# Kernel tuning notes

Hardware: AMD Instinct MI355X
Metric: run time of the kernel (lower is better)

## Reference

```python
import jax, jax.numpy as jnp
import numpy as np

B, T, Q, D = 8192, 65, 20, 100  # batch, tweet len, question len, 2*hidden_dim


def setup_inputs() -> dict:
    key = jax.random.key(0)
    kH, kU, k1, k2, k3 = jax.random.split(key, 5)
    # Ws params are a single normal row repeated across the length dim
    ws1 = jnp.tile(jax.random.normal(k1, (1, D), dtype=jnp.float32), (T, 1))
    ws2 = jnp.tile(jax.random.normal(k2, (1, D), dtype=jnp.float32), (Q, 1))
    ws3 = jnp.tile(jax.random.normal(k3, (1, D), dtype=jnp.float32), (T, 1))
    return {
        "H": jax.random.normal(kH, (B, T, D), dtype=jnp.float32),
        "U": jax.random.normal(kU, (B, Q, D), dtype=jnp.float32),
        "Ws1": ws1,
        "Ws2": ws2,
        "Ws3": ws3,
    }


def reference(H, U, Ws1, Ws2, Ws3):
    # H: [B,T,D], U: [B,Q,D]
    H1 = jnp.sum(H * Ws1, axis=2)[:, :, None]        # [B,T,1]
    U1 = jnp.sum(U * Ws2, axis=2)[:, None, :]        # [B,1,Q]
    HU = jnp.einsum('btd,bqd->btq', H * Ws3, U)      # [B,T,Q]
    S = H1 + U1 + HU                                 # [B,T,Q]
    at = jax.nn.softmax(S, axis=2)                   # attend tweet->question
    Util = jnp.einsum('btq,bqd->btd', at, U)         # [B,T,D]
    beta = jnp.max(S, axis=2)                        # [B,T]
    b = jax.nn.softmax(beta, axis=1)[:, :, None]     # [B,T,1]
    Htil = jnp.sum(b * H, axis=1)[:, None, :]        # [B,1,D] broadcast over T
    G = jnp.concatenate((H, Util, H * Util, H * Htil), axis=2)  # [B,T,4D]
    return G
```

## Files before the change

kernel.cpp:

```cpp
#include <hip/hip_runtime.h>
#include <math.h>

#define NB 8192
#define T 65
#define Q 20
#define D 100
#define D4 25
#define SP 24
#define SP4 6

__global__ __launch_bounds__(256) void attn_fused_kernel(
    const float* __restrict__ Hg,
    const float* __restrict__ Ug,
    const float* __restrict__ Ws1,
    const float* __restrict__ Ws2,
    const float* __restrict__ Ws3,
    float* __restrict__ Gg)
{
    __shared__ float4 sH4[T*D4];
    __shared__ float4 sU4[Q*D4];
    __shared__ float4 sU3e4[(Q+1)*D4];
    __shared__ float4 sS4[T*SP4];
    __shared__ float4 sHtilP[4][D4];
    __shared__ float4 sU1q4[5];
    __shared__ float  sH1[T];
    __shared__ float  sBeta[T];
    __shared__ float  sBsm[T];

    const int b   = blockIdx.x;
    const int tid = threadIdx.x;
    const float4* Hb = (const float4*)(Hg + (size_t)b * (T*D));
    const float4* Ub = (const float4*)(Ug + (size_t)b * (Q*D));
    float* sSf = (float*)sS4;

    for (int i = tid; i < T*D4; i += 256) sH4[i] = Hb[i];
    {
        const float4* w3g = (const float4*)Ws3;
        for (int i = tid; i < Q*D4; i += 256) {
            const float4 u = Ub[i];
            sU4[i] = u;
            const int dd = i - (i/D4)*D4;
            const float4 w = w3g[dd];
            float4 v; v.x=u.x*w.x; v.y=u.y*w.y; v.z=u.z*w.z; v.w=u.w*w.w;
            sU3e4[i] = v;
        }
        if (tid < D4) sU3e4[Q*D4 + tid] = ((const float4*)Ws1)[tid];
    }
    __syncthreads();

    if (tid < 119) {
        const int tg = tid / 7;
        const int jg = tid - tg*7;
        int rb0 = ((tg*4 + 0) < T ? (tg*4 + 0) : T-1) * D4;
        int rb1 = ((tg*4 + 1) < T ? (tg*4 + 1) : T-1) * D4;
        int rb2 = ((tg*4 + 2) < T ? (tg*4 + 2) : T-1) * D4;
        int rb3 = ((tg*4 + 3) < T ? (tg*4 + 3) : T-1) * D4;
        float acc[4][3];
        #pragma unroll
        for (int i = 0; i < 4; ++i)
            #pragma unroll
            for (int k = 0; k < 3; ++k) acc[i][k] = 0.f;
        #pragma unroll 5
        for (int d4 = 0; d4 < D4; ++d4) {
            float4 h0 = sH4[rb0 + d4];
            float4 h1 = sH4[rb1 + d4];
            float4 h2 = sH4[rb2 + d4];
            float4 h3 = sH4[rb3 + d4];
            #pragma unroll
            for (int k = 0; k < 3; ++k) {
                const float4 w = sU3e4[(jg*3+k)*D4 + d4];
                acc[0][k] = fmaf(h0.x, w.x, acc[0][k]); acc[0][k] = fmaf(h0.y, w.y, acc[0][k]);
                acc[0][k] = fmaf(h0.z, w.z, acc[0][k]); acc[0][k] = fmaf(h0.w, w.w, acc[0][k]);
                acc[1][k] = fmaf(h1.x, w.x, acc[1][k]); acc[1][k] = fmaf(h1.y, w.y, acc[1][k]);
                acc[1][k] = fmaf(h1.z, w.z, acc[1][k]); acc[1][k] = fmaf(h1.w, w.w, acc[1][k]);
                acc[2][k] = fmaf(h2.x, w.x, acc[2][k]); acc[2][k] = fmaf(h2.y, w.y, acc[2][k]);
                acc[2][k] = fmaf(h2.z, w.z, acc[2][k]); acc[2][k] = fmaf(h2.w, w.w, acc[2][k]);
                acc[3][k] = fmaf(h3.x, w.x, acc[3][k]); acc[3][k] = fmaf(h3.y, w.y, acc[3][k]);
                acc[3][k] = fmaf(h3.z, w.z, acc[3][k]); acc[3][k] = fmaf(h3.w, w.w, acc[3][k]);
            }
        }
        #pragma unroll
        for (int i = 0; i < 4; ++i) {
            const int t = tg*4 + i;
            if (t < T) {
                #pragma unroll
                for (int k = 0; k < 3; ++k) {
                    const int cc = jg*3 + k;
                    if (cc < Q) sSf[t*SP + cc] = acc[i][k];
                    else        sH1[t] = acc[i][k];
                }
            }
        }
    } else if (tid >= 128 && tid < 128 + Q) {
        const int q = tid - 128;
        const float4* ur = sU4 + q*D4;
        const float4* w2 = (const float4*)Ws2;
        float acc = 0.f;
        #pragma unroll
        for (int k = 0; k < D4; ++k) {
            const float4 u = ur[k], w = w2[k];
            acc = fmaf(u.x, w.x, acc); acc = fmaf(u.y, w.y, acc);
            acc = fmaf(u.z, w.z, acc); acc = fmaf(u.w, w.w, acc);
        }
        ((float*)sU1q4)[q] = acc;
    }
    __syncthreads();

    if (tid < T) {
        const int t = tid;
        float4 r[5];
        #pragma unroll
        for (int c = 0; c < 5; ++c) {
            r[c] = sS4[t*SP4 + c];
            const float4 u1 = sU1q4[c];
            r[c].x += u1.x; r[c].y += u1.y; r[c].z += u1.z; r[c].w += u1.w;
        }
        float m = -1e30f;
        #pragma unroll
        for (int c = 0; c < 5; ++c)
            m = fmaxf(m, fmaxf(fmaxf(r[c].x, r[c].y), fmaxf(r[c].z, r[c].w)));
        float s = 0.f;
        #pragma unroll
        for (int c = 0; c < 5; ++c) {
            r[c].x = __expf(r[c].x - m); r[c].y = __expf(r[c].y - m);
            r[c].z = __expf(r[c].z - m); r[c].w = __expf(r[c].w - m);
            s += r[c].x + r[c].y + r[c].z + r[c].w;
        }
        const float inv = 1.f / s;
        #pragma unroll
        for (int c = 0; c < 5; ++c) {
            r[c].x *= inv; r[c].y *= inv; r[c].z *= inv; r[c].w *= inv;
            sS4[t*SP4 + c] = r[c];
        }
        sBeta[t] = sH1[t] + m;
    }
    __syncthreads();

    if (tid < 64) {
        const float v0 = sBeta[tid];
        const float v1 = (tid == 0) ? sBeta[64] : -1e30f;
        float mx = fmaxf(v0, v1);
        #pragma unroll
        for (int off = 32; off >= 1; off >>= 1)
            mx = fmaxf(mx, __shfl_xor(mx, off, 64));
        const float e0 = __expf(v0 - mx);
        const float e1 = (tid == 0) ? __expf(v1 - mx) : 0.f;
        float s = e0 + e1;
        #pragma unroll
        for (int off = 32; off >= 1; off >>= 1)
            s += __shfl_xor(s, off, 64);
        const float inv = 1.f / s;
        sBsm[tid] = e0 * inv;
        if (tid == 0) sBsm[64] = e1 * inv;
    }
    __syncthreads();

    {
        const int wv = tid >> 6, lane = tid & 63;
        if (lane < D4) {
            float4 acc = {0.f, 0.f, 0.f, 0.f};
            for (int t = wv; t < T; t += 4) {
                const float bt = sBsm[t];
                const float4 h = sH4[t*D4 + lane];
                acc.x = fmaf(bt, h.x, acc.x); acc.y = fmaf(bt, h.y, acc.y);
                acc.z = fmaf(bt, h.z, acc.z); acc.w = fmaf(bt, h.w, acc.w);
            }
            sHtilP[wv][lane] = acc;
        }
    }
    __syncthreads();

    {
        const int wv   = tid >> 6;
        const int lane = tid & 63;
        const int tsel = (lane < 50) ? (lane / 25) : 0;
        const int g    = (lane < 50) ? (lane - tsel*25) : (lane - 50);
        const bool act = (lane < 50);
        float* Gb = Gg + (size_t)b * (T*4*D);

        const float4 p0 = sHtilP[0][g], p1 = sHtilP[1][g], p2 = sHtilP[2][g], p3 = sHtilP[3][g];
        float4 htil;
        htil.x = p0.x+p1.x+p2.x+p3.x; htil.y = p0.y+p1.y+p2.y+p3.y;
        htil.z = p0.z+p1.z+p2.z+p3.z; htil.w = p0.w+p1.w+p2.w+p3.w;

        float4 u[Q];
        #pragma unroll
        for (int q = 0; q < Q; ++q) u[q] = sU4[q*D4 + g];

        for (int pr = wv; pr < 33; pr += 4) {
            const int t   = pr*2 + tsel;
            const bool val = act && (t < T);
            const int tr  = val ? t : 0;

            const float4 a0 = sS4[tr*SP4 + 0];
            const float4 a1 = sS4[tr*SP4 + 1];
            const float4 a2 = sS4[tr*SP4 + 2];
            const float4 a3 = sS4[tr*SP4 + 3];
            const float4 a4 = sS4[tr*SP4 + 4];

            float4 acc = {0.f, 0.f, 0.f, 0.f};
            #define QSTEP(av, comp, qq) { \
                acc.x = fmaf(av.comp, u[qq].x, acc.x); \
                acc.y = fmaf(av.comp, u[qq].y, acc.y); \
                acc.z = fmaf(av.comp, u[qq].z, acc.z); \
                acc.w = fmaf(av.comp, u[qq].w, acc.w); }
            QSTEP(a0,x,0)  QSTEP(a0,y,1)  QSTEP(a0,z,2)  QSTEP(a0,w,3)
            QSTEP(a1,x,4)  QSTEP(a1,y,5)  QSTEP(a1,z,6)  QSTEP(a1,w,7)
            QSTEP(a2,x,8)  QSTEP(a2,y,9)  QSTEP(a2,z,10) QSTEP(a2,w,11)
            QSTEP(a3,x,12) QSTEP(a3,y,13) QSTEP(a3,z,14) QSTEP(a3,w,15)
            QSTEP(a4,x,16) QSTEP(a4,y,17) QSTEP(a4,z,18) QSTEP(a4,w,19)
            #undef QSTEP

            const float4 hv = sH4[tr*D4 + g];
            if (val) {
                float4 hu, hh;
                hu.x = hv.x*acc.x;  hu.y = hv.y*acc.y;  hu.z = hv.z*acc.z;  hu.w = hv.w*acc.w;
                hh.x = hv.x*htil.x; hh.y = hv.y*htil.y; hh.z = hv.z*htil.z; hh.w = hv.w*htil.w;
                float4* base = (float4*)(Gb + (size_t)t*(4*D));
                base[g]        = hv;
                base[D4 + g]   = acc;
                base[2*D4 + g] = hu;
                base[3*D4 + g] = hh;
            }
        }
    }
}

extern "C" void kernel_launch(void* const* d_in, const int* in_sizes, int n_in,
                              void* d_out, int out_size, void* d_ws, size_t ws_size,
                              hipStream_t stream) {
    const float* H   = (const float*)d_in[0];
    const float* U   = (const float*)d_in[1];
    const float* Ws1 = (const float*)d_in[2];
    const float* Ws2 = (const float*)d_in[3];
    const float* Ws3 = (const float*)d_in[4];
    float* G = (float*)d_out;
    hipLaunchKernelGGL(attn_fused_kernel, dim3(NB), dim3(256), 0, stream,
                       H, U, Ws1, Ws2, Ws3, G);
}
```

Baseline: 279.6 us.

## Shrink shared memory footprint and retile score GEMM for higher occupancy

Removes the shared copy of U and reads it from global/L2 instead, packs the score matrix without padding, and merges the three per-t scalar arrays into one buffer, so each block uses less LDS. It also sets launch_bounds to 4 blocks per CU. The score computation switches from 4 rows per thread on 119 threads to 8 rows per thread on 63 threads, which reuses each weight load across more rows. The Htil partial sums use 2 waves instead of 4. The risks are extra global traffic for U, more register pressure from 24 accumulators, and less parallelism in the score stage.

```diff
diff --git a/kernel.cpp b/kernel.cpp
--- a/kernel.cpp
+++ b/kernel.cpp
@@ -6,10 +6,9 @@
 #define Q 20
 #define D 100
 #define D4 25
-#define SP 24
-#define SP4 6
-
-__global__ __launch_bounds__(256) void attn_fused_kernel(
+#define SP4 5
+
+__global__ __launch_bounds__(256, 4) void attn_fused_kernel(
     const float* __restrict__ Hg,
     const float* __restrict__ Ug,
     const float* __restrict__ Ws1,
@@ -18,14 +17,11 @@
     float* __restrict__ Gg)
 {
     __shared__ float4 sH4[T*D4];
-    __shared__ float4 sU4[Q*D4];
     __shared__ float4 sU3e4[(Q+1)*D4];
     __shared__ float4 sS4[T*SP4];
-    __shared__ float4 sHtilP[4][D4];
+    __shared__ float4 sHtilP[2][D4];
     __shared__ float4 sU1q4[5];
-    __shared__ float  sH1[T];
-    __shared__ float  sBeta[T];
-    __shared__ float  sBsm[T];
+    __shared__ float  sScal[T];
 
     const int b   = blockIdx.x;
     const int tid = threadIdx.x;
@@ -38,7 +34,6 @@
         const float4* w3g = (const float4*)Ws3;
         for (int i = tid; i < Q*D4; i += 256) {
             const float4 u = Ub[i];
-            sU4[i] = u;
             const int dd = i - (i/D4)*D4;
             const float4 w = w3g[dd];
             float4 v; v.x=u.x*w.x; v.y=u.y*w.y; v.z=u.z*w.z; v.w=u.w*w.w;
@@ -48,52 +43,52 @@
     }
     __syncthreads();
 
-    if (tid < 119) {
+    if (tid < 63) {
         const int tg = tid / 7;
         const int jg = tid - tg*7;
-        int rb0 = ((tg*4 + 0) < T ? (tg*4 + 0) : T-1) * D4;
-        int rb1 = ((tg*4 + 1) < T ? (tg*4 + 1) : T-1) * D4;
-        int rb2 = ((tg*4 + 2) < T ? (tg*4 + 2) : T-1) * D4;
-        int rb3 = ((tg*4 + 3) < T ? (tg*4 + 3) : T-1) * D4;
-        float acc[4][3];
-        #pragma unroll
-        for (int i = 0; i < 4; ++i)
+        int rb[8];
+        #pragma unroll
+        for (int i = 0; i < 8; ++i) {
+            const int t = tg*8 + i;
+            rb[i] = ((t < T) ? t : T-1) * D4;
+        }
+        float acc[8][3];
+        #pragma unroll
+        for (int i = 0; i < 8; ++i)
             #pragma unroll
             for (int k = 0; k < 3; ++k) acc[i][k] = 0.f;
         #pragma unroll 5
         for (int d4 = 0; d4 < D4; ++d4) {
-            float4 h0 = sH4[rb0 + d4];
-            float4 h1 = sH4[rb1 + d4];
-            float4 h2 = sH4[rb2 + d4];
-            float4 h3 = sH4[rb3 + d4];
+            float4 w[3];
             #pragma unroll
-            for (int k = 0; k < 3; ++k) {
-                const float4 w = sU3e4[(jg*3+k)*D4 + d4];
-                acc[0][k] = fmaf(h0.x, w.x, acc[0][k]); acc[0][k] = fmaf(h0.y, w.y, acc[0][k]);
-                acc[0][k] = fmaf(h0.z, w.z, acc[0][k]); acc[0][k] = fmaf(h0.w, w.w, acc[0][k]);
-                acc[1][k] = fmaf(h1.x, w.x, acc[1][k]); acc[1][k] = fmaf(h1.y, w.y, acc[1][k]);
-                acc[1][k] = fmaf(h1.z, w.z, acc[1][k]); acc[1][k] = fmaf(h1.w, w.w, acc[1][k]);
-                acc[2][k] = fmaf(h2.x, w.x, acc[2][k]); acc[2][k] = fmaf(h2.y, w.y, acc[2][k]);
-                acc[2][k] = fmaf(h2.z, w.z, acc[2][k]); acc[2][k] = fmaf(h2.w, w.w, acc[2][k]);
-                acc[3][k] = fmaf(h3.x, w.x, acc[3][k]); acc[3][k] = fmaf(h3.y, w.y, acc[3][k]);
-                acc[3][k] = fmaf(h3.z, w.z, acc[3][k]); acc[3][k] = fmaf(h3.w, w.w, acc[3][k]);
-            }
-        }
-        #pragma unroll
-        for (int i = 0; i < 4; ++i) {
-            const int t = tg*4 + i;
+            for (int k = 0; k < 3; ++k) w[k] = sU3e4[(jg*3+k)*D4 + d4];
+            #pragma unroll
+            for (int i = 0; i < 8; ++i) {
+                const float4 h = sH4[rb[i] + d4];
+                #pragma unroll
+                for (int k = 0; k < 3; ++k) {
+                    acc[i][k] = fmaf(h.x, w[k].x, acc[i][k]);
+                    acc[i][k] = fmaf(h.y, w[k].y, acc[i][k]);
+                    acc[i][k] = fmaf(h.z, w[k].z, acc[i][k]);
+                    acc[i][k] = fmaf(h.w, w[k].w, acc[i][k]);
+                }
+            }
+        }
+        #pragma unroll
+        for (int i = 0; i < 8; ++i) {
+            const int t = tg*8 + i;
             if (t < T) {
                 #pragma unroll
                 for (int k = 0; k < 3; ++k) {
                     const int cc = jg*3 + k;
-                    if (cc < Q) sSf[t*SP + cc] = acc[i][k];
-                    else        sH1[t] = acc[i][k];
+                    if (cc < Q) sSf[t*Q + cc] = acc[i][k];
+                    else        sScal[t] = acc[i][k];
                 }
             }
         }
-    } else if (tid >= 128 && tid < 128 + Q) {
-        const int q = tid - 128;
-        const float4* ur = sU4 + q*D4;
+    } else if (tid >= 64 && tid < 64 + Q) {
+        const int q = tid - 64;
+        const float4* ur = Ub + q*D4;
         const float4* w2 = (const float4*)Ws2;
         float acc = 0.f;
         #pragma unroll
@@ -108,37 +103,37 @@
 
     if (tid < T) {
         const int t = tid;
-        float4 r[5];
-        #pragma unroll
-        for (int c = 0; c < 5; ++c) {
+        float4 r[SP4];
+        #pragma unroll
+        for (int c = 0; c < SP4; ++c) {
             r[c] = sS4[t*SP4 + c];
             const float4 u1 = sU1q4[c];
             r[c].x += u1.x; r[c].y += u1.y; r[c].z += u1.z; r[c].w += u1.w;
         }
         float m = -1e30f;
         #pragma unroll
-        for (int c = 0; c < 5; ++c)
+        for (int c = 0; c < SP4; ++c)
             m = fmaxf(m, fmaxf(fmaxf(r[c].x, r[c].y), fmaxf(r[c].z, r[c].w)));
         float s = 0.f;
         #pragma unroll
-        for (int c = 0; c < 5; ++c) {
+        for (int c = 0; c < SP4; ++c) {
             r[c].x = __expf(r[c].x - m); r[c].y = __expf(r[c].y - m);
             r[c].z = __expf(r[c].z - m); r[c].w = __expf(r[c].w - m);
             s += r[c].x + r[c].y + r[c].z + r[c].w;
         }
         const float inv = 1.f / s;
         #pragma unroll
-        for (int c = 0; c < 5; ++c) {
+        for (int c = 0; c < SP4; ++c) {
             r[c].x *= inv; r[c].y *= inv; r[c].z *= inv; r[c].w *= inv;
             sS4[t*SP4 + c] = r[c];
         }
-        sBeta[t] = sH1[t] + m;
+        sScal[t] = sScal[t] + m;
     }
     __syncthreads();
 
     if (tid < 64) {
-        const float v0 = sBeta[tid];
-        const float v1 = (tid == 0) ? sBeta[64] : -1e30f;
+        const float v0 = sScal[tid];
+        const float v1 = (tid == 0) ? sScal[64] : -1e30f;
         float mx = fmaxf(v0, v1);
         #pragma unroll
         for (int off = 32; off >= 1; off >>= 1)
@@ -150,17 +145,17 @@
         for (int off = 32; off >= 1; off >>= 1)
             s += __shfl_xor(s, off, 64);
         const float inv = 1.f / s;
-        sBsm[tid] = e0 * inv;
-        if (tid == 0) sBsm[64] = e1 * inv;
+        sScal[tid] = e0 * inv;
+        if (tid == 0) sScal[64] = e1 * inv;
     }
     __syncthreads();
 
     {
         const int wv = tid >> 6, lane = tid & 63;
-        if (lane < D4) {
+        if (wv < 2 && lane < D4) {
             float4 acc = {0.f, 0.f, 0.f, 0.f};
-            for (int t = wv; t < T; t += 4) {
-                const float bt = sBsm[t];
+            for (int t = wv; t < T; t += 2) {
+                const float bt = sScal[t];
                 const float4 h = sH4[t*D4 + lane];
                 acc.x = fmaf(bt, h.x, acc.x); acc.y = fmaf(bt, h.y, acc.y);
                 acc.z = fmaf(bt, h.z, acc.z); acc.w = fmaf(bt, h.w, acc.w);
@@ -178,15 +173,15 @@
         const bool act = (lane < 50);
         float* Gb = Gg + (size_t)b * (T*4*D);
 
-        const float4 p0 = sHtilP[0][g], p1 = sHtilP[1][g], p2 = sHtilP[2][g], p3 = sHtilP[3][g];
+        const float4 p0 = sHtilP[0][g], p1 = sHtilP[1][g];
         float4 htil;
-        htil.x = p0.x+p1.x+p2.x+p3.x; htil.y = p0.y+p1.y+p2.y+p3.y;
-        htil.z = p0.z+p1.z+p2.z+p3.z; htil.w = p0.w+p1.w+p2.w+p3.w;
+        htil.x = p0.x+p1.x; htil.y = p0.y+p1.y; htil.z = p0.z+p1.z; htil.w = p0.w+p1.w;
 
         float4 u[Q];
         #pragma unroll
-        for (int q = 0; q < Q; ++q) u[q] = sU4[q*D4 + g];
-
+        for (int q = 0; q < Q; ++q) u[q] = Ub[q*D4 + g];
+
+        #pragma unroll 1
         for (int pr = wv; pr < 33; pr += 4) {
             const int t   = pr*2 + tsel;
             const bool val = act && (t < T);
```

New measurement: 365.7 us. 1.31x slower.
